# Kernel tuning notes

Hardware: AMD Instinct MI355X
Metric: run time of the kernel (lower is better)

The kernel has to match this reference:

```python
import jax, jax.numpy as jnp
import numpy as np

N = 50000   # nodes
E = 800000  # edges
F = 256     # in_channels
H = 256     # hidden (GCN output)


def setup_inputs() -> dict:
    key = jax.random.key(0)
    ks = jax.random.split(key, 6)
    x = jax.random.normal(ks[0], (N, F), jnp.float32)
    edge_index = jax.random.randint(ks[1], (2, E), 0, N)
    perm = jax.random.permutation(ks[2], N)
    W = jax.random.normal(ks[3], (F, H), jnp.float32) / np.sqrt(F)
    b = jnp.zeros((H,), jnp.float32)
    a = jnp.full((1,), 0.25, jnp.float32)  # PReLU slope
    disc_W = jax.random.normal(ks[4], (H, H), jnp.float32) / np.sqrt(H)
    return {"x": x, "W": W, "b": b, "a": a, "disc_W": disc_W,
            "edge_index": edge_index, "perm": perm}


def _gcn(x, W, b, src, dst, n):
    # GCNConv: linear -> symmetric-normalized aggregation (with self-loops) -> bias
    xw = x @ W  # [N, H]
    loop = jnp.arange(n)
    s = jnp.concatenate([src, loop])
    d = jnp.concatenate([dst, loop])
    ew = jnp.ones(s.shape[0], xw.dtype)
    deg = jax.ops.segment_sum(ew, d, num_segments=n)          # [N]
    dinv = jnp.where(deg > 0, jax.lax.rsqrt(deg), 0.0)
    norm = dinv[s] * dinv[d]                                   # [E+N]
    out = jax.ops.segment_sum(xw[s] * norm[:, None], d, num_segments=n)
    return out + b


def reference(x, W, b, a, disc_W, edge_index, perm):
    src, dst = edge_index[0], edge_index[1]
    n = x.shape[0]

    def encode(feat):
        h = _gcn(feat, W, b, src, dst, n)
        return jnp.where(h >= 0, h, a * h)  # PReLU

    z1 = encode(x)          # clean
    z2 = encode(x[perm])    # corrupted (row permutation)
    summary = jax.nn.sigmoid(z1.mean(axis=0))  # [H]
    wsum = disc_W @ summary                     # [H]
    pos = z1 @ wsum  # [N]
    neg = z2 @ wsum  # [N]
    return pos, neg
```

## Files before the change

kernel.cpp:

```cpp
#include <hip/hip_runtime.h>

#define N_NODES 50000
#define N_EDGES 800000
#define DIM 256
#define NB 196
#define UNROLL 8
#define MAXE (N_EDGES + N_NODES * UNROLL)
#define CSB 512
#define NCH 8
#define CCOLS 32
#define CHSZ (N_NODES * CCOLS)
#define RPB 16
#define CHB (N_NODES / RPB)

typedef __attribute__((ext_vector_type(8))) short bf16x8;
typedef __attribute__((ext_vector_type(4))) float f32x4;

__device__ __forceinline__ unsigned int f2bf(float f) {
  unsigned int u = __float_as_uint(f);
  return (u + 0x7FFFu + ((u >> 16) & 1u)) >> 16;
}
__device__ __forceinline__ float bf_lo(unsigned int u) {
  return __uint_as_float(u << 16);
}
__device__ __forceinline__ float bf_hi(unsigned int u) {
  return __uint_as_float(u & 0xFFFF0000u);
}


__global__ void k_deg(const int* __restrict__ dst, int* __restrict__ deg) {
  int e = blockIdx.x * blockDim.x + threadIdx.x;
  if (e < N_EDGES) atomicAdd(&deg[dst[e]], 1);
}

__global__ __launch_bounds__(256) void k_bsum(const int* __restrict__ deg,
                                              float* __restrict__ dinv,
                                              int* __restrict__ bsum) {
  __shared__ int red[4];
  const int t = threadIdx.x;
  const int i = blockIdx.x * 256 + t;
  int pd = 0;
  if (i < N_NODES) {
    int d = deg[i];
    dinv[i] = rsqrtf((float)(d + 1));
    pd = (d + UNROLL - 1) & ~(UNROLL - 1);
  }
  int s = pd;
#pragma unroll
  for (int off = 32; off > 0; off >>= 1) s += __shfl_down(s, off);
  if ((t & 63) == 0) red[t >> 6] = s;
  __syncthreads();
  if (t == 0) bsum[blockIdx.x] = red[0] + red[1] + red[2] + red[3];
}

__global__ __launch_bounds__(256) void k_bscan(const int* __restrict__ bsum,
                                               int* __restrict__ boff,
                                               int* __restrict__ row_start) {
  __shared__ int s[256];
  const int t = threadIdx.x;
  int v = (t < NB) ? bsum[t] : 0;
  s[t] = v;
  __syncthreads();
  for (int off = 1; off < 256; off <<= 1) {
    int u = (t >= off) ? s[t - off] : 0;
    __syncthreads();
    s[t] += u;
    __syncthreads();
  }
  if (t < NB) boff[t] = s[t] - v;
  if (t == NB - 1) row_start[N_NODES] = s[NB - 1];
}

__global__ __launch_bounds__(256) void k_rowstart(const int* __restrict__ deg,
                                                  const int* __restrict__ boff,
                                                  int* __restrict__ row_start,
                                                  int* __restrict__ cursor) {
  __shared__ int s[256];
  const int t = threadIdx.x;
  const int i = blockIdx.x * 256 + t;
  int pd = (i < N_NODES) ? ((deg[i] + UNROLL - 1) & ~(UNROLL - 1)) : 0;
  s[t] = pd;
  __syncthreads();
  for (int off = 1; off < 256; off <<= 1) {
    int u = (t >= off) ? s[t - off] : 0;
    __syncthreads();
    s[t] += u;
    __syncthreads();
  }
  if (i < N_NODES) {
    int r = boff[blockIdx.x] + s[t] - pd;
    row_start[i] = r;
    cursor[i] = r;
  }
}

__global__ void k_scatter(const int* __restrict__ src, const int* __restrict__ dst,
                          const int* __restrict__ perm, const float* __restrict__ dinv,
                          int* __restrict__ cursor, uint2* __restrict__ meta) {
  int e = blockIdx.x * blockDim.x + threadIdx.x;
  if (e < N_EDGES) {
    int s = src[e], d = dst[e];
    int p = atomicAdd(&cursor[d], 1);
    meta[p] = make_uint2((unsigned)s | ((unsigned)perm[s] << 16),
                         __float_as_uint(dinv[s] * dinv[d]));
  }
}


__global__ void k_prep(const float* __restrict__ W, ushort* __restrict__ Wt) {
  int n = blockIdx.x, k = threadIdx.x;
  Wt[n * DIM + k] = (ushort)f2bf(W[k * DIM + n]);
}


__global__ __launch_bounds__(512) void k_gemm(const float* __restrict__ X,
                                              const ushort* __restrict__ Wt,
                                              ushort* __restrict__ XWC) {
  __shared__ ushort Xs[128 * 40];
  __shared__ ushort Ws[256 * 40];
  const int tid = threadIdx.x;
  const int lane = tid & 63;
  const int w = tid >> 6;
  const int wm = w >> 2, wn = w & 3;
  const int m0 = blockIdx.x * 128;
  const int l16 = lane & 15, kh = lane >> 4;

  f32x4 acc[4][4];
#pragma unroll
  for (int mf = 0; mf < 4; ++mf)
#pragma unroll
    for (int nf = 0; nf < 4; ++nf) acc[mf][nf] = (f32x4){0.f, 0.f, 0.f, 0.f};

  for (int k0 = 0; k0 < DIM; k0 += 32) {
#pragma unroll
    for (int it = 0; it < 2; ++it) {
      int idx = tid + it * 512;
      int row = idx >> 3, q = idx & 7;
      int grow = m0 + row;
      float4 v = make_float4(0.f, 0.f, 0.f, 0.f);
      if (grow < N_NODES)
        v = *reinterpret_cast<const float4*>(&X[(size_t)grow * DIM + k0 + q * 4]);
      uint2 p;
      p.x = f2bf(v.x) | (f2bf(v.y) << 16);
      p.y = f2bf(v.z) | (f2bf(v.w) << 16);
      *reinterpret_cast<uint2*>(&Xs[row * 40 + q * 4]) = p;
    }
#pragma unroll
    for (int it = 0; it < 2; ++it) {
      int idx = tid + it * 512;
      int n = idx >> 2, c = idx & 3;
      uint4 wv = *reinterpret_cast<const uint4*>(&Wt[n * DIM + k0 + c * 8]);
      *reinterpret_cast<uint4*>(&Ws[n * 40 + c * 8]) = wv;
    }
    __syncthreads();
    bf16x8 a[4], b[4];
#pragma unroll
    for (int f = 0; f < 4; ++f) {
      a[f] = *reinterpret_cast<const bf16x8*>(&Ws[(wn * 64 + f * 16 + l16) * 40 + kh * 8]);
      b[f] = *reinterpret_cast<const bf16x8*>(&Xs[(wm * 64 + f * 16 + l16) * 40 + kh * 8]);
    }
#pragma unroll
    for (int mf = 0; mf < 4; ++mf)
#pragma unroll
      for (int nf = 0; nf < 4; ++nf)
        acc[mf][nf] = __builtin_amdgcn_mfma_f32_16x16x32_bf16(a[nf], b[mf],
                                                              acc[mf][nf], 0, 0, 0);
    __syncthreads();
  }
#pragma unroll
  for (int mf = 0; mf < 4; ++mf) {
    int m = m0 + wm * 64 + mf * 16 + l16;
    if (m >= N_NODES) continue;
#pragma unroll
    for (int nf = 0; nf < 4; ++nf) {
      int nb = wn * 64 + nf * 16 + kh * 4;
      uint2 p;
      p.x = f2bf(acc[mf][nf][0]) | (f2bf(acc[mf][nf][1]) << 16);
      p.y = f2bf(acc[mf][nf][2]) | (f2bf(acc[mf][nf][3]) << 16);
      *reinterpret_cast<uint2*>(&XWC[(size_t)(nb >> 5) * CHSZ + (size_t)m * CCOLS + (nb & 31)]) = p;
    }
  }
}


__device__ __forceinline__ void fma8(float* A, uint4 v, float n) {
  A[0] = fmaf(bf_lo(v.x), n, A[0]);
  A[1] = fmaf(bf_hi(v.x), n, A[1]);
  A[2] = fmaf(bf_lo(v.y), n, A[2]);
  A[3] = fmaf(bf_hi(v.y), n, A[3]);
  A[4] = fmaf(bf_lo(v.z), n, A[4]);
  A[5] = fmaf(bf_hi(v.z), n, A[5]);
  A[6] = fmaf(bf_lo(v.w), n, A[6]);
  A[7] = fmaf(bf_hi(v.w), n, A[7]);
}

__global__ __launch_bounds__(256) void k_aggc(
    const ushort* __restrict__ xwc, const int* __restrict__ row_start,
    const uint2* __restrict__ meta, const int* __restrict__ perm,
    const float* __restrict__ dinv, const float* __restrict__ bias,
    const float* __restrict__ slope, ushort* __restrict__ z1,
    ushort* __restrict__ z2) {
  const int blk = blockIdx.x;
  const int ch = blk / CHB;
  const int rb = blk % CHB;
  const int tid = threadIdx.x;
  const int r = rb * RPB + (tid >> 4);
  const int l = tid & 15;
  const int eg = l >> 2;
  const int sc = l & 3;
  const ushort* xc = xwc + (size_t)ch * CHSZ;

  float a1[8] = {0.f, 0.f, 0.f, 0.f, 0.f, 0.f, 0.f, 0.f};
  float a2[8] = {0.f, 0.f, 0.f, 0.f, 0.f, 0.f, 0.f, 0.f};
  const int e1 = row_start[r + 1];
  for (int e = row_start[r]; e < e1; e += 8) {
    uint4 mm = *reinterpret_cast<const uint4*>(meta + e + eg * 2);
    uint4 vA1 = *reinterpret_cast<const uint4*>(xc + (size_t)(mm.x & 0xFFFFu) * CCOLS + sc * 8);
    uint4 vA2 = *reinterpret_cast<const uint4*>(xc + (size_t)(mm.x >> 16) * CCOLS + sc * 8);
    uint4 vB1 = *reinterpret_cast<const uint4*>(xc + (size_t)(mm.z & 0xFFFFu) * CCOLS + sc * 8);
    uint4 vB2 = *reinterpret_cast<const uint4*>(xc + (size_t)(mm.z >> 16) * CCOLS + sc * 8);
    const float nA = __uint_as_float(mm.y), nB = __uint_as_float(mm.w);
    fma8(a1, vA1, nA); fma8(a2, vA2, nA);
    fma8(a1, vB1, nB); fma8(a2, vB2, nB);
  }
#pragma unroll
  for (int j = 0; j < 8; ++j) {
    a1[j] += __shfl_xor(a1[j], 4); a2[j] += __shfl_xor(a2[j], 4);
    a1[j] += __shfl_xor(a1[j], 8); a2[j] += __shfl_xor(a2[j], 8);
  }
  if (eg == 0) {
    const float di = dinv[r];
    const float d2 = di * di;
    const int pr = perm[r];
    uint4 s1 = *reinterpret_cast<const uint4*>(xc + (size_t)r * CCOLS + sc * 8);
    uint4 s2 = *reinterpret_cast<const uint4*>(xc + (size_t)pr * CCOLS + sc * 8);
    fma8(a1, s1, d2); fma8(a2, s2, d2);
    const float* bp = bias + ch * CCOLS + sc * 8;
    float4 b0 = *reinterpret_cast<const float4*>(bp);
    float4 b1 = *reinterpret_cast<const float4*>(bp + 4);
    a1[0] += b0.x; a1[1] += b0.y; a1[2] += b0.z; a1[3] += b0.w;
    a1[4] += b1.x; a1[5] += b1.y; a1[6] += b1.z; a1[7] += b1.w;
    a2[0] += b0.x; a2[1] += b0.y; a2[2] += b0.z; a2[3] += b0.w;
    a2[4] += b1.x; a2[5] += b1.y; a2[6] += b1.z; a2[7] += b1.w;
    const float a0 = slope[0];
#pragma unroll
    for (int j = 0; j < 8; ++j) {
      a1[j] = a1[j] >= 0.f ? a1[j] : a0 * a1[j];
      a2[j] = a2[j] >= 0.f ? a2[j] : a0 * a2[j];
    }
    uint4 p1, p2;
    p1.x = f2bf(a1[0]) | (f2bf(a1[1]) << 16);
    p1.y = f2bf(a1[2]) | (f2bf(a1[3]) << 16);
    p1.z = f2bf(a1[4]) | (f2bf(a1[5]) << 16);
    p1.w = f2bf(a1[6]) | (f2bf(a1[7]) << 16);
    p2.x = f2bf(a2[0]) | (f2bf(a2[1]) << 16);
    p2.y = f2bf(a2[2]) | (f2bf(a2[3]) << 16);
    p2.z = f2bf(a2[4]) | (f2bf(a2[5]) << 16);
    p2.w = f2bf(a2[6]) | (f2bf(a2[7]) << 16);
    const size_t o = (size_t)r * DIM + ch * CCOLS + sc * 8;
    *reinterpret_cast<uint4*>(z1 + o) = p1;
    *reinterpret_cast<uint4*>(z2 + o) = p2;
  }
}


__global__ __launch_bounds__(256) void k_colsum(const ushort* __restrict__ z1,
                                                float* __restrict__ partial) {
  __shared__ float red[8 * 256];
  const int t = threadIdx.x;
  const int c8 = t & 31;
  const int g = t >> 5;
  float s[8] = {0.f, 0.f, 0.f, 0.f, 0.f, 0.f, 0.f, 0.f};
  for (int r = blockIdx.x * 8 + g; r < N_NODES; r += 8 * CSB) {
    uint4 v = *reinterpret_cast<const uint4*>(z1 + (size_t)r * DIM + c8 * 8);
    s[0] += bf_lo(v.x); s[1] += bf_hi(v.x);
    s[2] += bf_lo(v.y); s[3] += bf_hi(v.y);
    s[4] += bf_lo(v.z); s[5] += bf_hi(v.z);
    s[6] += bf_lo(v.w); s[7] += bf_hi(v.w);
  }
#pragma unroll
  for (int j = 0; j < 8; ++j) red[g * 256 + c8 * 8 + j] = s[j];
  __syncthreads();
  float tot = 0.f;
#pragma unroll
  for (int g2 = 0; g2 < 8; ++g2) tot += red[g2 * 256 + t];
  partial[blockIdx.x * 256 + t] = tot;
}

__global__ __launch_bounds__(256) void k_wsum(const float* __restrict__ partial,
                                              const float* __restrict__ disc_W,
                                              float* __restrict__ wsum) {
  __shared__ float s[DIM];
  const int t = threadIdx.x;
  float a0 = 0.f, a1 = 0.f, a2 = 0.f, a3 = 0.f;
  for (int b = 0; b < CSB; b += 4) {
    a0 += partial[(b + 0) * 256 + t];
    a1 += partial[(b + 1) * 256 + t];
    a2 += partial[(b + 2) * 256 + t];
    a3 += partial[(b + 3) * 256 + t];
  }
  float m = (a0 + a1 + a2 + a3) * (1.0f / (float)N_NODES);
  s[t] = 1.0f / (1.0f + expf(-m));
  __syncthreads();
  float acc = 0.f;
  for (int j = 0; j < DIM; j += 4) {
    float4 w4 = *reinterpret_cast<const float4*>(&disc_W[t * DIM + j]);
    acc += w4.x * s[j] + w4.y * s[j + 1] + w4.z * s[j + 2] + w4.w * s[j + 3];
  }
  wsum[t] = acc;
}


__global__ __launch_bounds__(256) void k_posneg(const ushort* __restrict__ z1,
                                                const ushort* __restrict__ z2,
                                                const float* __restrict__ wsum,
                                                float* __restrict__ pos,
                                                float* __restrict__ neg) {
  const int wid = (blockIdx.x * blockDim.x + threadIdx.x) >> 6;
  const int lane = threadIdx.x & 63;
  if (wid >= N_NODES) return;
  uint2 v1 = *reinterpret_cast<const uint2*>(z1 + (size_t)wid * DIM + lane * 4);
  uint2 v2 = *reinterpret_cast<const uint2*>(z2 + (size_t)wid * DIM + lane * 4);
  float4 w4 = *reinterpret_cast<const float4*>(&wsum[lane * 4]);
  float dp = bf_lo(v1.x) * w4.x + bf_hi(v1.x) * w4.y + bf_lo(v1.y) * w4.z + bf_hi(v1.y) * w4.w;
  float dn = bf_lo(v2.x) * w4.x + bf_hi(v2.x) * w4.y + bf_lo(v2.y) * w4.z + bf_hi(v2.y) * w4.w;
#pragma unroll
  for (int off = 32; off > 0; off >>= 1) {
    dp += __shfl_down(dp, off);
    dn += __shfl_down(dn, off);
  }
  if (lane == 0) { pos[wid] = dp; neg[wid] = dn; }
}


extern "C" void kernel_launch(void* const* d_in, const int* in_sizes, int n_in,
                              void* d_out, int out_size, void* d_ws, size_t ws_size,
                              hipStream_t stream) {
  const float* x      = (const float*)d_in[0];
  const float* W      = (const float*)d_in[1];
  const float* b      = (const float*)d_in[2];
  const float* a      = (const float*)d_in[3];
  const float* disc_W = (const float*)d_in[4];
  const int*   eidx   = (const int*)d_in[5];
  const int*   perm   = (const int*)d_in[6];
  const int* src = eidx;
  const int* dst = eidx + N_EDGES;

  constexpr size_t SZ_BFM  = (size_t)N_NODES * DIM * 2;
  constexpr size_t SZ_META = (size_t)MAXE * 8;
  constexpr size_t OFF_XWC = 0;
  constexpr size_t OFF_Z1  = OFF_XWC + SZ_BFM;
  constexpr size_t OFF_Z2  = OFF_Z1 + SZ_BFM;
  constexpr size_t OFF_WT  = OFF_Z2 + SZ_BFM;
  constexpr size_t OFF_DEG = OFF_WT + 131072;
  constexpr size_t OFF_DNV = OFF_DEG + 200192;
  constexpr size_t OFF_RS  = OFF_DNV + 200192;
  constexpr size_t OFF_CUR = OFF_RS + 200448;
  constexpr size_t OFF_MT  = OFF_CUR + 200192;
  constexpr size_t OFF_WSM = OFF_MT + SZ_META;
  constexpr size_t OFF_BS  = OFF_WSM + 1024;
  constexpr size_t OFF_BO  = OFF_BS + 1024;
  constexpr size_t OFF_PT  = OFF_BO + 1024;
  constexpr size_t NEED    = OFF_PT + (size_t)CSB * 256 * 4;
  if (ws_size < NEED) return;

  char* ws = (char*)d_ws;
  ushort* xwc    = (ushort*)(ws + OFF_XWC);
  ushort* z1     = (ushort*)(ws + OFF_Z1);
  ushort* z2     = (ushort*)(ws + OFF_Z2);
  ushort* Wt     = (ushort*)(ws + OFF_WT);
  int*    deg    = (int*)(ws + OFF_DEG);
  float*  dinv   = (float*)(ws + OFF_DNV);
  int*    rowst  = (int*)(ws + OFF_RS);
  int*    cursor = (int*)(ws + OFF_CUR);
  uint2*  meta   = (uint2*)(ws + OFF_MT);
  float*  wsum   = (float*)(ws + OFF_WSM);
  int*    bsum   = (int*)(ws + OFF_BS);
  int*    boff   = (int*)(ws + OFF_BO);
  float*  partial= (float*)(ws + OFF_PT);

  float* pos = (float*)d_out;
  float* neg = pos + N_NODES;

  hipMemsetAsync(deg, 0, N_NODES * sizeof(int), stream);
  hipMemsetAsync(meta, 0, SZ_META, stream);

  k_deg<<<(N_EDGES + 255) / 256, 256, 0, stream>>>(dst, deg);
  k_bsum<<<NB, 256, 0, stream>>>(deg, dinv, bsum);
  k_bscan<<<1, 256, 0, stream>>>(bsum, boff, rowst);
  k_rowstart<<<NB, 256, 0, stream>>>(deg, boff, rowst, cursor);
  k_scatter<<<(N_EDGES + 255) / 256, 256, 0, stream>>>(src, dst, perm, dinv,
                                                       cursor, meta);

  k_prep<<<DIM, DIM, 0, stream>>>(W, Wt);
  k_gemm<<<(N_NODES + 127) / 128, 512, 0, stream>>>(x, Wt, xwc);

  k_aggc<<<NCH * CHB, 256, 0, stream>>>(xwc, rowst, meta, perm, dinv, b, a, z1, z2);

  k_colsum<<<CSB, 256, 0, stream>>>(z1, partial);
  k_wsum<<<1, 256, 0, stream>>>(partial, disc_W, wsum);
  k_posneg<<<(N_NODES * 64 + 255) / 256, 256, 0, stream>>>(z1, z2, wsum, pos, neg);
}
```

Before: 247.5 us.

## Widen XW column chunks to 64 and use packed float2 FMAs in aggregation

Changes the chunked XW layout from 8 chunks of 32 columns to 4 chunks of 64 columns, so each gathered neighbor row segment is 128 bytes and half as many chunk passes re-read the edge metadata. The aggregation thread mapping becomes 2 edge groups by 8 column slices, each thread handling 4 edge pairs per iteration and needing only one shuffle reduction step. Accumulation switches to float2 vector ops, which the compiler may lower to packed FMA, and addresses use 32-bit shifts. The cost is more loads in flight per thread and fewer blocks in the aggregation grid.

```diff
diff --git a/kernel.cpp b/kernel.cpp
--- a/kernel.cpp
+++ b/kernel.cpp
@@ -7,14 +7,15 @@
 #define UNROLL 8
 #define MAXE (N_EDGES + N_NODES * UNROLL)
 #define CSB 512
-#define NCH 8
-#define CCOLS 32
+#define NCH 4
+#define CCOLS 64
 #define CHSZ (N_NODES * CCOLS)
 #define RPB 16
 #define CHB (N_NODES / RPB)
 
 typedef __attribute__((ext_vector_type(8))) short bf16x8;
 typedef __attribute__((ext_vector_type(4))) float f32x4;
+typedef __attribute__((ext_vector_type(2))) float f32x2;
 
 __device__ __forceinline__ unsigned int f2bf(float f) {
   unsigned int u = __float_as_uint(f);
@@ -177,21 +178,18 @@
       uint2 p;
       p.x = f2bf(acc[mf][nf][0]) | (f2bf(acc[mf][nf][1]) << 16);
       p.y = f2bf(acc[mf][nf][2]) | (f2bf(acc[mf][nf][3]) << 16);
-      *reinterpret_cast<uint2*>(&XWC[(size_t)(nb >> 5) * CHSZ + (size_t)m * CCOLS + (nb & 31)]) = p;
+      *reinterpret_cast<uint2*>(
+          &XWC[(size_t)(nb >> 6) * CHSZ + (size_t)m * CCOLS + (nb & 63)]) = p;
     }
   }
 }
 
 
-__device__ __forceinline__ void fma8(float* A, uint4 v, float n) {
-  A[0] = fmaf(bf_lo(v.x), n, A[0]);
-  A[1] = fmaf(bf_hi(v.x), n, A[1]);
-  A[2] = fmaf(bf_lo(v.y), n, A[2]);
-  A[3] = fmaf(bf_hi(v.y), n, A[3]);
-  A[4] = fmaf(bf_lo(v.z), n, A[4]);
-  A[5] = fmaf(bf_hi(v.z), n, A[5]);
-  A[6] = fmaf(bf_lo(v.w), n, A[6]);
-  A[7] = fmaf(bf_hi(v.w), n, A[7]);
+__device__ __forceinline__ void fma8v(f32x2* A, uint4 v, f32x2 n) {
+  A[0] += (f32x2){bf_lo(v.x), bf_hi(v.x)} * n;
+  A[1] += (f32x2){bf_lo(v.y), bf_hi(v.y)} * n;
+  A[2] += (f32x2){bf_lo(v.z), bf_hi(v.z)} * n;
+  A[3] += (f32x2){bf_lo(v.w), bf_hi(v.w)} * n;
 }
 
 __global__ __launch_bounds__(256) void k_aggc(
@@ -206,57 +204,72 @@
   const int tid = threadIdx.x;
   const int r = rb * RPB + (tid >> 4);
   const int l = tid & 15;
-  const int eg = l >> 2;
-  const int sc = l & 3;
+  const int eg = l >> 3;
+  const int sc = l & 7;
   const ushort* xc = xwc + (size_t)ch * CHSZ;
-
-  float a1[8] = {0.f, 0.f, 0.f, 0.f, 0.f, 0.f, 0.f, 0.f};
-  float a2[8] = {0.f, 0.f, 0.f, 0.f, 0.f, 0.f, 0.f, 0.f};
+  const unsigned scb = sc * 8;
+
+  f32x2 a1[4] = {{0.f, 0.f}, {0.f, 0.f}, {0.f, 0.f}, {0.f, 0.f}};
+  f32x2 a2[4] = {{0.f, 0.f}, {0.f, 0.f}, {0.f, 0.f}, {0.f, 0.f}};
   const int e1 = row_start[r + 1];
   for (int e = row_start[r]; e < e1; e += 8) {
-    uint4 mm = *reinterpret_cast<const uint4*>(meta + e + eg * 2);
-    uint4 vA1 = *reinterpret_cast<const uint4*>(xc + (size_t)(mm.x & 0xFFFFu) * CCOLS + sc * 8);
-    uint4 vA2 = *reinterpret_cast<const uint4*>(xc + (size_t)(mm.x >> 16) * CCOLS + sc * 8);
-    uint4 vB1 = *reinterpret_cast<const uint4*>(xc + (size_t)(mm.z & 0xFFFFu) * CCOLS + sc * 8);
-    uint4 vB2 = *reinterpret_cast<const uint4*>(xc + (size_t)(mm.z >> 16) * CCOLS + sc * 8);
-    const float nA = __uint_as_float(mm.y), nB = __uint_as_float(mm.w);
-    fma8(a1, vA1, nA); fma8(a2, vA2, nA);
-    fma8(a1, vB1, nB); fma8(a2, vB2, nB);
-  }
-#pragma unroll
-  for (int j = 0; j < 8; ++j) {
-    a1[j] += __shfl_xor(a1[j], 4); a2[j] += __shfl_xor(a2[j], 4);
-    a1[j] += __shfl_xor(a1[j], 8); a2[j] += __shfl_xor(a2[j], 8);
+    uint4 m0 = *reinterpret_cast<const uint4*>(meta + e + eg * 2);
+    uint4 m1 = *reinterpret_cast<const uint4*>(meta + e + 4 + eg * 2);
+    uint4 vA1 = *reinterpret_cast<const uint4*>(xc + ((m0.x & 0xFFFFu) << 6) + scb);
+    uint4 vA2 = *reinterpret_cast<const uint4*>(xc + ((m0.x >> 16) << 6) + scb);
+    uint4 vB1 = *reinterpret_cast<const uint4*>(xc + ((m0.z & 0xFFFFu) << 6) + scb);
+    uint4 vB2 = *reinterpret_cast<const uint4*>(xc + ((m0.z >> 16) << 6) + scb);
+    uint4 vC1 = *reinterpret_cast<const uint4*>(xc + ((m1.x & 0xFFFFu) << 6) + scb);
+    uint4 vC2 = *reinterpret_cast<const uint4*>(xc + ((m1.x >> 16) << 6) + scb);
+    uint4 vD1 = *reinterpret_cast<const uint4*>(xc + ((m1.z & 0xFFFFu) << 6) + scb);
+    uint4 vD2 = *reinterpret_cast<const uint4*>(xc + ((m1.z >> 16) << 6) + scb);
+    const float fA = __uint_as_float(m0.y), fB = __uint_as_float(m0.w);
+    const float fC = __uint_as_float(m1.y), fD = __uint_as_float(m1.w);
+    const f32x2 nA = {fA, fA}, nB = {fB, fB}, nC = {fC, fC}, nD = {fD, fD};
+    fma8v(a1, vA1, nA); fma8v(a2, vA2, nA);
+    fma8v(a1, vB1, nB); fma8v(a2, vB2, nB);
+    fma8v(a1, vC1, nC); fma8v(a2, vC2, nC);
+    fma8v(a1, vD1, nD); fma8v(a2, vD2, nD);
+  }
+#pragma unroll
+  for (int j = 0; j < 4; ++j) {
+    a1[j].x += __shfl_xor(a1[j].x, 8);
+    a1[j].y += __shfl_xor(a1[j].y, 8);
+    a2[j].x += __shfl_xor(a2[j].x, 8);
+    a2[j].y += __shfl_xor(a2[j].y, 8);
   }
   if (eg == 0) {
     const float di = dinv[r];
     const float d2 = di * di;
+    const f32x2 nd = {d2, d2};
     const int pr = perm[r];
-    uint4 s1 = *reinterpret_cast<const uint4*>(xc + (size_t)r * CCOLS + sc * 8);
-    uint4 s2 = *reinterpret_cast<const uint4*>(xc + (size_t)pr * CCOLS + sc * 8);
-    fma8(a1, s1, d2); fma8(a2, s2, d2);
+    uint4 s1 = *reinterpret_cast<const uint4*>(xc + ((unsigned)r << 6) + scb);
+    uint4 s2 = *reinterpret_cast<const uint4*>(xc + ((unsigned)pr << 6) + scb);
+    fma8v(a1, s1, nd); fma8v(a2, s2, nd);
     const float* bp = bias + ch * CCOLS + sc * 8;
     float4 b0 = *reinterpret_cast<const float4*>(bp);
     float4 b1 = *reinterpret_cast<const float4*>(bp + 4);
-    a1[0] += b0.x; a1[1] += b0.y; a1[2] += b0.z; a1[3] += b0.w;
-    a1[4] += b1.x; a1[5] += b1.y; a1[6] += b1.z; a1[7] += b1.w;
-    a2[0] += b0.x; a2[1] += b0.y; a2[2] += b0.z; a2[3] += b0.w;
-    a2[4] += b1.x; a2[5] += b1.y; a2[6] += b1.z; a2[7] += b1.w;
+    a1[0] += (f32x2){b0.x, b0.y}; a1[1] += (f32x2){b0.z, b0.w};
+    a1[2] += (f32x2){b1.x, b1.y}; a1[3] += (f32x2){b1.z, b1.w};
+    a2[0] += (f32x2){b0.x, b0.y}; a2[1] += (f32x2){b0.z, b0.w};
+    a2[2] += (f32x2){b1.x, b1.y}; a2[3] += (f32x2){b1.z, b1.w};
     const float a0 = slope[0];
 #pragma unroll
-    for (int j = 0; j < 8; ++j) {
-      a1[j] = a1[j] >= 0.f ? a1[j] : a0 * a1[j];
-      a2[j] = a2[j] >= 0.f ? a2[j] : a0 * a2[j];
+    for (int j = 0; j < 4; ++j) {
+      a1[j].x = a1[j].x >= 0.f ? a1[j].x : a0 * a1[j].x;
+      a1[j].y = a1[j].y >= 0.f ? a1[j].y : a0 * a1[j].y;
+      a2[j].x = a2[j].x >= 0.f ? a2[j].x : a0 * a2[j].x;
+      a2[j].y = a2[j].y >= 0.f ? a2[j].y : a0 * a2[j].y;
     }
     uint4 p1, p2;
-    p1.x = f2bf(a1[0]) | (f2bf(a1[1]) << 16);
-    p1.y = f2bf(a1[2]) | (f2bf(a1[3]) << 16);
-    p1.z = f2bf(a1[4]) | (f2bf(a1[5]) << 16);
-    p1.w = f2bf(a1[6]) | (f2bf(a1[7]) << 16);
-    p2.x = f2bf(a2[0]) | (f2bf(a2[1]) << 16);
-    p2.y = f2bf(a2[2]) | (f2bf(a2[3]) << 16);
-    p2.z = f2bf(a2[4]) | (f2bf(a2[5]) << 16);
-    p2.w = f2bf(a2[6]) | (f2bf(a2[7]) << 16);
+    p1.x = f2bf(a1[0].x) | (f2bf(a1[0].y) << 16);
+    p1.y = f2bf(a1[1].x) | (f2bf(a1[1].y) << 16);
+    p1.z = f2bf(a1[2].x) | (f2bf(a1[2].y) << 16);
+    p1.w = f2bf(a1[3].x) | (f2bf(a1[3].y) << 16);
+    p2.x = f2bf(a2[0].x) | (f2bf(a2[0].y) << 16);
+    p2.y = f2bf(a2[1].x) | (f2bf(a2[1].y) << 16);
+    p2.z = f2bf(a2[2].x) | (f2bf(a2[2].y) << 16);
+    p2.w = f2bf(a2[3].x) | (f2bf(a2[3].y) << 16);
     const size_t o = (size_t)r * DIM + ch * CCOLS + sc * 8;
     *reinterpret_cast<uint4*>(z1 + o) = p1;
     *reinterpret_cast<uint4*>(z2 + o) = p2;
```

After: 236.4 us. 1.05x faster.
